# Kernel tuning notes

Hardware: AMD Instinct MI355X
Metric: run time of the kernel (lower is better)

The kernel has to match this reference:

```python
import jax, jax.numpy as jnp
import numpy as np

BN, BE, B = 50000, 800000, 16
NE, EE, GE, EH, NH = 32, 32, 32, 128, 128  # emb dims, hidden dims


def clean(x):
    return jnp.nan_to_num(x, nan=0.0, posinf=0.0, neginf=0.0)


def _lin(key, fan_in, fan_out):
    k1, k2 = jax.random.split(key)
    s = 1.0 / np.sqrt(fan_in)
    return (jax.random.uniform(k1, (fan_in, fan_out), jnp.float32, -s, s),
            jax.random.uniform(k2, (fan_out,), jnp.float32, -s, s))


def setup_inputs() -> dict:
    key = jax.random.key(0)
    ks = jax.random.split(key, 20)
    inp = {
        "x": jax.random.normal(ks[0], (BN, 2), jnp.float32),
        "edge_index": jax.random.randint(ks[1], (2, BE), 0, BN, jnp.int32),
        "batch": jax.random.randint(ks[2], (BN,), 0, B, jnp.int32),
        "node_attr": jnp.ones((BN, 2), jnp.float32),
        "edge_attr": jax.random.uniform(ks[3], (BE, 2), jnp.float32) + 0.5,  # positive spacings
        "glob_attr": jax.random.uniform(ks[4], (B, 2), jnp.float32),
    }
    # encoders (output 2*emb each, 'Duplicated')
    inp["enc_node_W"], inp["enc_node_b"] = _lin(ks[5], 2, 2 * NE)
    inp["enc_edge_W"], inp["enc_edge_b"] = _lin(ks[6], 2, 2 * EE)
    inp["enc_glob_W"], inp["enc_glob_b"] = _lin(ks[7], 2, 2 * GE)
    inp["enc2_W"], inp["enc2_b"] = _lin(ks[8], 2, 2 * EE)
    # derivative MLP: 4*NE+2*EE -> EH -> 2*EE
    inp["dW1"], inp["db1"] = _lin(ks[9], 4 * NE + 2 * EE, EH)
    inp["dW2"], inp["db2"] = _lin(ks[10], EH, 2 * EE)
    # half-jacobian MLP: 4*EE -> EH -> 2*EE
    inp["hW1"], inp["hb1"] = _lin(ks[11], 4 * EE, EH)
    inp["hW2"], inp["hb2"] = _lin(ks[12], EH, 2 * EE)
    # jacobian MLP: 6*EE -> NH -> 2*NE
    inp["jW1"], inp["jb1"] = _lin(ks[13], 6 * EE, NH)
    inp["jW2"], inp["jb2"] = _lin(ks[14], NH, 2 * NE)
    # hessian MLP: 4*EE+2*EE -> NH -> 2*NE
    inp["sW1"], inp["sb1"] = _lin(ks[15], 6 * EE, NH)
    inp["sW2"], inp["sb2"] = _lin(ks[16], NH, 2 * NE)
    # node MLP: 6*NE+2*GE -> NH -> 2*NE
    inp["nW1"], inp["nb1"] = _lin(ks[17], 6 * NE + 2 * GE, NH)
    inp["nW2"], inp["nb2"] = _lin(ks[18], NH, 2 * NE)
    # decoder: 2*NE -> 2
    inp["decW"], inp["decb"] = _lin(ks[19], 2 * NE, 2)
    return inp


def reference(x, edge_index, batch, node_attr, edge_attr, glob_attr,
              enc_node_W, enc_node_b, enc_edge_W, enc_edge_b, enc_glob_W, enc_glob_b,
              enc2_W, enc2_b,
              dW1, db1, dW2, db2,
              hW1, hb1, hW2, hb2,
              jW1, jb1, jW2, jb2,
              sW1, sb1, sW2, sb2,
              nW1, nb1, nW2, nb2,
              decW, decb):
    relu = jax.nn.relu
    seg = lambda d, idx: jax.ops.segment_sum(d, idx, num_segments=BN)
    mlp = lambda t, W1, b1, W2, b2: relu(t @ W1 + b1) @ W2 + b2

    row, col = edge_index[0], edge_index[1]
    spacing = edge_attr                                 # [BE,2]
    inv_spacing = clean(1.0 / spacing)
    inv_double = clean(1.0 / (seg(spacing, row) + seg(spacing, col)))  # [BN,2]

    node_emb = relu(x @ enc_node_W + enc_node_b)        # [BN,2*NE]
    spacing_emb = relu(spacing @ enc_edge_W + enc_edge_b)  # [BE,2*EE]
    glob_emb = relu(glob_attr @ enc_glob_W + enc_glob_b)   # [B,2*GE]
    inv_spacing_emb = relu(inv_spacing @ enc2_W + enc2_b)  # [BE,2*EE]
    inv_double_emb = relu(inv_double @ enc2_W + enc2_b)    # [BN,2*EE]

    d_edge = mlp(jnp.concatenate([node_emb[row], node_emb[col], inv_spacing_emb], -1),
                 dW1, db1, dW2, db2)                    # [BE,2*EE]
    hj_plus = seg(d_edge, row)                          # [BN,2*EE]
    hj_minus = seg(d_edge, col)

    jac1 = seg(mlp(jnp.concatenate([spacing_emb, hj_plus[col]], -1), hW1, hb1, hW2, hb2), col)
    jac2 = seg(mlp(jnp.concatenate([spacing_emb, hj_minus[row]], -1), hW1, hb1, hW2, hb2), row)
    jac = mlp(jnp.concatenate([jac1, jac2, inv_double_emb], -1), jW1, jb1, jW2, jb2)  # [BN,2*NE]

    hess = mlp(jnp.concatenate([hj_plus, hj_minus, inv_double_emb], -1), sW1, sb1, sW2, sb2)

    res = mlp(jnp.concatenate([node_emb, jac, glob_emb[batch], hess], -1), nW1, nb1, nW2, nb2)
    return node_attr * (res @ decW + decb)              # [BN,2]
```

## Files before the change

### kernel.cpp

```cpp
#include <hip/hip_runtime.h>
#include <hip/hip_fp16.h>
#include <math.h>

#define BN 50000
#define BE 800000
#define CHUNK 104

typedef _Float16 h2 __attribute__((ext_vector_type(2)));

__device__ __forceinline__ float relu_f(float v) { return fmaxf(v, 0.0f); }
__device__ __forceinline__ float inv_clean(float s) {
    float q = 1.0f / s;
    return isfinite(q) ? q : 0.0f;
}
__device__ __forceinline__ float inv_clean_fast(float s) {
    float q = __builtin_amdgcn_rcpf(s);
    return isfinite(q) ? q : 0.0f;
}
__device__ __forceinline__ float fdot2f(h2 a, h2 b, float c) {
    return __builtin_amdgcn_fdot2(a, b, c, false);
}
__device__ __forceinline__ unsigned int h2u(h2 v) { union { h2 h; unsigned int u; } x; x.h = v; return x.u; }
__device__ __forceinline__ h2 uh2(unsigned int v) { union { unsigned int u; h2 h; } x; x.u = v; return x.h; }
__device__ __forceinline__ unsigned int packh2(float a, float b) {
    h2 h; h.x = (_Float16)a; h.y = (_Float16)b; return h2u(h);
}

__global__ __launch_bounds__(256) void k_pack_w1(
    const float* __restrict__ W, int r0, float4* __restrict__ dst)
{
    int t = blockIdx.x * 256 + threadIdx.x;
    if (t >= 2048) return;
    int j2 = t >> 6, l = t & 63;
    const float* ra = W + (size_t)(r0 + 2*j2) * 128 + 2*l;
    const float* rb = W + (size_t)(r0 + 2*j2 + 1) * 128 + 2*l;
    dst[t] = make_float4(ra[0], ra[1], rb[0], rb[1]);
}
__global__ __launch_bounds__(256) void k_pack_uv(
    const float* __restrict__ dW1, float4* __restrict__ dst)
{
    int t = blockIdx.x * 256 + threadIdx.x;
    if (t >= 4096) return;
    int j = t >> 6, l = t & 63;
    float4 w;
    if (l < 32) w = ((const float4*)(dW1 + (size_t)j*128))[l];
    else        w = ((const float4*)(dW1 + (size_t)(64+j)*128))[l-32];
    dst[t] = w;
}
__global__ __launch_bounds__(256) void k_pack_w1h(
    const float* __restrict__ W, int r0, uint2* __restrict__ dst)
{
    int t = blockIdx.x * 256 + threadIdx.x;
    if (t >= 2048) return;
    int j2 = t >> 6, l = t & 63;
    const float* ra = W + (size_t)(r0 + 2*j2) * 128;
    const float* rb = W + (size_t)(r0 + 2*j2 + 1) * 128;
    dst[t] = make_uint2(packh2(ra[2*l],   rb[2*l]),
                        packh2(ra[2*l+1], rb[2*l+1]));
}
__global__ __launch_bounds__(256) void k_pack_w2h(
    const float* __restrict__ W2, uint2* __restrict__ dst)
{
    int t = blockIdx.x * 256 + threadIdx.x;
    if (t >= 2048) return;
    int k4 = t >> 6, l = t & 63;
    dst[t] = make_uint2(packh2(W2[(4*k4+0)*64+l], W2[(4*k4+1)*64+l]),
                        packh2(W2[(4*k4+2)*64+l], W2[(4*k4+3)*64+l]));
}

__global__ __launch_bounds__(256) void k_hist(
    const int* __restrict__ ei, int* __restrict__ rc, int* __restrict__ cc)
{
    int e = blockIdx.x * 256 + threadIdx.x;
    if (e >= BE) return;
    atomicAdd(&rc[ei[e]], 1);
    atomicAdd(&cc[ei[BE + e]], 1);
}

__global__ __launch_bounds__(1024) void k_scan(
    const int* __restrict__ cntR, int* __restrict__ hdR,
    const int* __restrict__ cntC, int* __restrict__ hdC)
{
    __shared__ int s[1024];
    const int* cnt; int* hd;
    if (blockIdx.x == 0) { cnt = cntR; hd = hdR; }
    else                 { cnt = cntC; hd = hdC; }
    int t = threadIdx.x;
    int base = t * 49;
    int sum = 0;
    for (int i = 0; i < 49; i++) {
        int idx = base + i;
        sum += (idx < BN) ? cnt[idx] : 0;
    }
    s[t] = sum;
    __syncthreads();
    for (int o = 1; o < 1024; o <<= 1) {
        int v = (t >= o) ? s[t - o] : 0;
        __syncthreads();
        s[t] += v;
        __syncthreads();
    }
    int run = s[t] - sum;
    for (int i = 0; i < 49; i++) {
        int idx = base + i;
        if (idx < BN) { hd[idx] = run; run += cnt[idx]; }
    }
}

__global__ __launch_bounds__(256) void k_scatter2(
    const int* __restrict__ ei, const float* __restrict__ ea,
    int* __restrict__ rhd, int* __restrict__ chd,
    int4* __restrict__ rs, int4* __restrict__ cs)
{
    int e = blockIdx.x * 256 + threadIdx.x;
    if (e >= BE) return;
    int r = ei[e], c = ei[BE + e];
    float2 s = ((const float2*)ea)[e];
    int s0 = __float_as_int(s.x), s1 = __float_as_int(s.y);
    int p1 = atomicAdd(&rhd[r], 1);
    rs[p1] = make_int4(r, c, s0, s1);
    int p2 = atomicAdd(&chd[c], 1);
    cs[p2] = make_int4(c, r, s0, s1);
}

__global__ __launch_bounds__(256) void k_sumsp2(
    const int4* __restrict__ rs, const int* __restrict__ rhd, const int* __restrict__ rcnt,
    const int4* __restrict__ cs, const int* __restrict__ chd, const int* __restrict__ ccnt,
    float* __restrict__ sumsp)
{
    int n = blockIdx.x * 256 + threadIdx.x;
    if (n >= BN) return;
    float s0 = 0.f, s1 = 0.f;
    int e1 = rhd[n], e0 = e1 - rcnt[n];
    for (int j = e0; j < e1; j++) {
        int4 rec = rs[j];
        s0 += __int_as_float(rec.z); s1 += __int_as_float(rec.w);
    }
    e1 = chd[n]; e0 = e1 - ccnt[n];
    for (int j = e0; j < e1; j++) {
        int4 rec = cs[j];
        s0 += __int_as_float(rec.z); s1 += __int_as_float(rec.w);
    }
    sumsp[2*n]   = s0;
    sumsp[2*n+1] = s1;
}

__global__ __launch_bounds__(256, 6) void k_uvh(
    const float* __restrict__ x,
    const float* __restrict__ enW, const float* __restrict__ enB,
    const float4* __restrict__ guv,
    __half* __restrict__ u_h, __half* __restrict__ v_h)
{
    extern __shared__ float lds[];
    const int wid = threadIdx.x >> 6, l = threadIdx.x & 63;
    float4* xb4 = (float4*)(lds + wid * 512);
    const int gw = blockIdx.x * 4 + wid;
    const int nw = gridDim.x * 4;

    const int jj = l & 31;
    const float w0a = enW[jj],    w0b = enW[64+jj],  b0 = enB[jj];
    const float w1a = enW[jj+32], w1b = enW[96+jj],  b1 = enB[jj+32];

    for (int g = gw; g < BN/8; g += nw) {
        const int n0 = g * 8;
        const int q = l >> 5;
        {
            float2 xa = ((const float2*)x)[n0 + q*4 + 0];
            float2 xb = ((const float2*)x)[n0 + q*4 + 1];
            float2 xc = ((const float2*)x)[n0 + q*4 + 2];
            float2 xd = ((const float2*)x)[n0 + q*4 + 3];
            float4 p0, p1;
            p0.x = relu_f(fmaf(xa.x, w0a, fmaf(xa.y, w0b, b0)));
            p0.y = relu_f(fmaf(xb.x, w0a, fmaf(xb.y, w0b, b0)));
            p0.z = relu_f(fmaf(xc.x, w0a, fmaf(xc.y, w0b, b0)));
            p0.w = relu_f(fmaf(xd.x, w0a, fmaf(xd.y, w0b, b0)));
            p1.x = relu_f(fmaf(xa.x, w1a, fmaf(xa.y, w1b, b1)));
            p1.y = relu_f(fmaf(xb.x, w1a, fmaf(xb.y, w1b, b1)));
            p1.z = relu_f(fmaf(xc.x, w1a, fmaf(xc.y, w1b, b1)));
            p1.w = relu_f(fmaf(xd.x, w1a, fmaf(xd.y, w1b, b1)));
            xb4[jj*2 + q]      = p0;
            xb4[(jj+32)*2 + q] = p1;
        }
        float4 acc[8];
        #pragma unroll
        for (int e = 0; e < 8; e++) acc[e] = make_float4(0,0,0,0);
        #pragma unroll 8
        for (int j = 0; j < 64; j++) {
            float4 wq = guv[j*64 + l];
            float4 xa = xb4[j*2 + 0];
            float4 xc = xb4[j*2 + 1];
            acc[0].x = fmaf(xa.x, wq.x, acc[0].x); acc[0].y = fmaf(xa.x, wq.y, acc[0].y);
            acc[0].z = fmaf(xa.x, wq.z, acc[0].z); acc[0].w = fmaf(xa.x, wq.w, acc[0].w);
            acc[1].x = fmaf(xa.y, wq.x, acc[1].x); acc[1].y = fmaf(xa.y, wq.y, acc[1].y);
            acc[1].z = fmaf(xa.y, wq.z, acc[1].z); acc[1].w = fmaf(xa.y, wq.w, acc[1].w);
            acc[2].x = fmaf(xa.z, wq.x, acc[2].x); acc[2].y = fmaf(xa.z, wq.y, acc[2].y);
            acc[2].z = fmaf(xa.z, wq.z, acc[2].z); acc[2].w = fmaf(xa.z, wq.w, acc[2].w);
            acc[3].x = fmaf(xa.w, wq.x, acc[3].x); acc[3].y = fmaf(xa.w, wq.y, acc[3].y);
            acc[3].z = fmaf(xa.w, wq.z, acc[3].z); acc[3].w = fmaf(xa.w, wq.w, acc[3].w);
            acc[4].x = fmaf(xc.x, wq.x, acc[4].x); acc[4].y = fmaf(xc.x, wq.y, acc[4].y);
            acc[4].z = fmaf(xc.x, wq.z, acc[4].z); acc[4].w = fmaf(xc.x, wq.w, acc[4].w);
            acc[5].x = fmaf(xc.y, wq.x, acc[5].x); acc[5].y = fmaf(xc.y, wq.y, acc[5].y);
            acc[5].z = fmaf(xc.y, wq.z, acc[5].z); acc[5].w = fmaf(xc.y, wq.w, acc[5].w);
            acc[6].x = fmaf(xc.z, wq.x, acc[6].x); acc[6].y = fmaf(xc.z, wq.y, acc[6].y);
            acc[6].z = fmaf(xc.z, wq.z, acc[6].z); acc[6].w = fmaf(xc.z, wq.w, acc[6].w);
            acc[7].x = fmaf(xc.w, wq.x, acc[7].x); acc[7].y = fmaf(xc.w, wq.y, acc[7].y);
            acc[7].z = fmaf(xc.w, wq.z, acc[7].z); acc[7].w = fmaf(xc.w, wq.w, acc[7].w);
        }
        __half* dst = (l < 32) ? (u_h + 4*l) : (v_h + 4*(l-32));
        #pragma unroll
        for (int e = 0; e < 8; e++) {
            __half2* p = (__half2*)(dst + (size_t)(n0+e)*128);
            p[0] = __floats2half2_rn(acc[e].x, acc[e].y);
            p[1] = __floats2half2_rn(acc[e].z, acc[e].w);
        }
    }
}

__global__ __launch_bounds__(256, 8) void k_e1d(
    const int4* __restrict__ recs,
    const __half* __restrict__ A_h, const __half* __restrict__ B_h,
    const float* __restrict__ e2w, const float* __restrict__ e2b,
    const uint2* __restrict__ pw1, const float* __restrict__ db1,
    const uint2* __restrict__ pw2, const float* __restrict__ db2,
    float* __restrict__ outAcc)
{
    extern __shared__ unsigned int ldsu[];
    const int wid = threadIdx.x >> 6, l = threadIdx.x & 63;
    uint4* xbuf = (uint4*)ldsu + (size_t)wid * 192;
    uint4* hbuf = xbuf + 64;

    const int j2 = l >> 1, eh = l & 1;
    const float w0a = e2w[2*j2],    w0b = e2w[64+2*j2], eb0 = e2b[2*j2];
    const float w1a = e2w[2*j2+1],  w1b = e2w[65+2*j2], eb1 = e2b[2*j2+1];
    const float b1a = db1[2*l], b1b = db1[2*l+1];
    const float b2r = db2[l];

    const int wave = blockIdx.x * 4 + wid;
    const int start = wave * CHUNK;
    const int end = min(start + CHUNK, BE);

    float acc = 0.f;
    int cur = -1;

    for (int i = start; i < end; i += 8) {
        const int nact = min(8, end - i);
        int key[8], oth[8];
        float spx[8], spy[8];
        #pragma unroll
        for (int e = 0; e < 8; e++) {
            int idx = i + ((e < nact) ? e : nact - 1);
            int4 rec = recs[idx];
            key[e] = rec.x; oth[e] = rec.y;
            spx[e] = __int_as_float(rec.z); spy[e] = __int_as_float(rec.w);
        }
        {
            uint4 xw;
            unsigned int* xp = (unsigned int*)&xw;
            #pragma unroll
            for (int c = 0; c < 4; c++) {
                int e = 4*eh + c;
                float q0 = inv_clean_fast(spx[e]);
                float q1 = inv_clean_fast(spy[e]);
                float r0 = relu_f(fmaf(q0, w0a, fmaf(q1, w0b, eb0)));
                float r1 = relu_f(fmaf(q0, w1a, fmaf(q1, w1b, eb1)));
                xp[c] = packh2(r0, r1);
            }
            xbuf[j2*2 + eh] = xw;
        }
        float t0[8], t1[8];
        #pragma unroll
        for (int e = 0; e < 8; e++) {
            float2 au = __half22float2(*(const __half2*)(A_h + (size_t)key[e]*128 + 2*l));
            float2 bu = __half22float2(*(const __half2*)(B_h + (size_t)oth[e]*128 + 2*l));
            t0[e] = b1a + au.x + bu.x;
            t1[e] = b1b + au.y + bu.y;
        }
        #pragma unroll 8
        for (int p = 0; p < 32; p++) {
            uint4 x0 = xbuf[p*2 + 0];
            uint4 x1 = xbuf[p*2 + 1];
            uint2 wv = pw1[p*64 + l];
            h2 wa = uh2(wv.x), wb = uh2(wv.y);
            t0[0] = fdot2f(uh2(x0.x), wa, t0[0]); t1[0] = fdot2f(uh2(x0.x), wb, t1[0]);
            t0[1] = fdot2f(uh2(x0.y), wa, t0[1]); t1[1] = fdot2f(uh2(x0.y), wb, t1[1]);
            t0[2] = fdot2f(uh2(x0.z), wa, t0[2]); t1[2] = fdot2f(uh2(x0.z), wb, t1[2]);
            t0[3] = fdot2f(uh2(x0.w), wa, t0[3]); t1[3] = fdot2f(uh2(x0.w), wb, t1[3]);
            t0[4] = fdot2f(uh2(x1.x), wa, t0[4]); t1[4] = fdot2f(uh2(x1.x), wb, t1[4]);
            t0[5] = fdot2f(uh2(x1.y), wa, t0[5]); t1[5] = fdot2f(uh2(x1.y), wb, t1[5]);
            t0[6] = fdot2f(uh2(x1.z), wa, t0[6]); t1[6] = fdot2f(uh2(x1.z), wb, t1[6]);
            t0[7] = fdot2f(uh2(x1.w), wa, t0[7]); t1[7] = fdot2f(uh2(x1.w), wb, t1[7]);
        }
        {
            uint4 hA, hB;
            unsigned int* pa = (unsigned int*)&hA;
            unsigned int* pb = (unsigned int*)&hB;
            #pragma unroll
            for (int c = 0; c < 4; c++) {
                pa[c] = packh2(relu_f(t0[c]),   relu_f(t1[c]));
                pb[c] = packh2(relu_f(t0[4+c]), relu_f(t1[4+c]));
            }
            hbuf[l*2 + 0] = hA;
            hbuf[l*2 + 1] = hB;
        }
        float o[8] = {0,0,0,0,0,0,0,0};
        #pragma unroll 8
        for (int k4 = 0; k4 < 32; k4++) {
            uint4 a0 = hbuf[(2*k4)*2 + 0];
            uint4 a1 = hbuf[(2*k4)*2 + 1];
            uint4 b0 = hbuf[(2*k4+1)*2 + 0];
            uint4 b1 = hbuf[(2*k4+1)*2 + 1];
            uint2 wv = pw2[k4*64 + l];
            h2 wa = uh2(wv.x), wb = uh2(wv.y);
            o[0] = fdot2f(uh2(b0.x), wb, fdot2f(uh2(a0.x), wa, o[0]));
            o[1] = fdot2f(uh2(b0.y), wb, fdot2f(uh2(a0.y), wa, o[1]));
            o[2] = fdot2f(uh2(b0.z), wb, fdot2f(uh2(a0.z), wa, o[2]));
            o[3] = fdot2f(uh2(b0.w), wb, fdot2f(uh2(a0.w), wa, o[3]));
            o[4] = fdot2f(uh2(b1.x), wb, fdot2f(uh2(a1.x), wa, o[4]));
            o[5] = fdot2f(uh2(b1.y), wb, fdot2f(uh2(a1.y), wa, o[5]));
            o[6] = fdot2f(uh2(b1.z), wb, fdot2f(uh2(a1.z), wa, o[6]));
            o[7] = fdot2f(uh2(b1.w), wb, fdot2f(uh2(a1.w), wa, o[7]));
        }
        #pragma unroll
        for (int e = 0; e < 8; e++) {
            if (e < nact) {
                float val = o[e] + b2r;
                if (key[e] != cur) {
                    if (cur >= 0) atomicAdd(&outAcc[(size_t)cur*64 + l], acc);
                    acc = 0.f;
                    cur = key[e];
                }
                acc += val;
            }
        }
    }
    if (cur >= 0) atomicAdd(&outAcc[(size_t)cur*64 + l], acc);
}

__global__ __launch_bounds__(256, 6) void k_tptmh(
    const float* __restrict__ hjp, const float* __restrict__ hjm,
    const float4* __restrict__ gtp,
    __half* __restrict__ tp_h, __half* __restrict__ tm_h)
{
    extern __shared__ float lds[];
    const int wid = threadIdx.x >> 6, l = threadIdx.x & 63;
    float4* xb4 = (float4*)(lds + wid * 512);
    const int gw = blockIdx.x * 4 + wid;
    const int nw = gridDim.x * 4;
    const int NG = BN/8;

    for (int vg = gw; vg < 2*NG; vg += nw) {
        const float* in = (vg < NG) ? hjp : hjm;
        __half*     out = (vg < NG) ? tp_h : tm_h;
        const int n0 = ((vg < NG) ? vg : vg - NG) * 8;
        const int q = l >> 5;
        #pragma unroll
        for (int r = 0; r < 2; r++) {
            int j = (l & 31) + 32*r;
            float v0 = in[(n0 + q*4 + 0)*64 + j];
            float v1 = in[(n0 + q*4 + 1)*64 + j];
            float v2 = in[(n0 + q*4 + 2)*64 + j];
            float v3 = in[(n0 + q*4 + 3)*64 + j];
            xb4[j*2 + q] = make_float4(v0, v1, v2, v3);
        }
        float a0[8] = {0,0,0,0,0,0,0,0}, a1[8] = {0,0,0,0,0,0,0,0};
        #pragma unroll 8
        for (int j2 = 0; j2 < 32; j2++) {
            float4 wq = gtp[j2*64 + l];
            float4 xa = xb4[(2*j2)*2 + 0];
            float4 xbv = xb4[(2*j2)*2 + 1];
            float4 xc = xb4[(2*j2+1)*2 + 0];
            float4 xd = xb4[(2*j2+1)*2 + 1];
            a0[0] = fmaf(xa.x, wq.x, fmaf(xc.x, wq.z, a0[0]));
            a1[0] = fmaf(xa.x, wq.y, fmaf(xc.x, wq.w, a1[0]));
            a0[1] = fmaf(xa.y, wq.x, fmaf(xc.y, wq.z, a0[1]));
            a1[1] = fmaf(xa.y, wq.y, fmaf(xc.y, wq.w, a1[1]));
            a0[2] = fmaf(xa.z, wq.x, fmaf(xc.z, wq.z, a0[2]));
            a1[2] = fmaf(xa.z, wq.y, fmaf(xc.z, wq.w, a1[2]));
            a0[3] = fmaf(xa.w, wq.x, fmaf(xc.w, wq.z, a0[3]));
            a1[3] = fmaf(xa.w, wq.y, fmaf(xc.w, wq.w, a1[3]));
            a0[4] = fmaf(xbv.x, wq.x, fmaf(xd.x, wq.z, a0[4]));
            a1[4] = fmaf(xbv.x, wq.y, fmaf(xd.x, wq.w, a1[4]));
            a0[5] = fmaf(xbv.y, wq.x, fmaf(xd.y, wq.z, a0[5]));
            a1[5] = fmaf(xbv.y, wq.y, fmaf(xd.y, wq.w, a1[5]));
            a0[6] = fmaf(xbv.z, wq.x, fmaf(xd.z, wq.z, a0[6]));
            a1[6] = fmaf(xbv.z, wq.y, fmaf(xd.z, wq.w, a1[6]));
            a0[7] = fmaf(xbv.w, wq.x, fmaf(xd.w, wq.z, a0[7]));
            a1[7] = fmaf(xbv.w, wq.y, fmaf(xd.w, wq.w, a1[7]));
        }
        #pragma unroll
        for (int e = 0; e < 8; e++) {
            *(__half2*)(out + (size_t)(n0+e)*128 + 2*l) = __floats2half2_rn(a0[e], a1[e]);
        }
    }
}

__global__ __launch_bounds__(256, 8) void k_e2s(
    const int4* __restrict__ recs, const __half* __restrict__ tvals_h,
    const float* __restrict__ eew, const float* __restrict__ eeb,
    const uint2* __restrict__ pw1, const float* __restrict__ hb1,
    const uint2* __restrict__ pw2, const float* __restrict__ hb2,
    float* __restrict__ out)
{
    extern __shared__ unsigned int ldsu[];
    const int wid = threadIdx.x >> 6, l = threadIdx.x & 63;
    uint4* xbuf = (uint4*)ldsu + (size_t)wid * 192;
    uint4* hbuf = xbuf + 64;

    const int j2 = l >> 1, eh = l & 1;
    const float w0a = eew[2*j2],    w0b = eew[64+2*j2], eb0 = eeb[2*j2];
    const float w1a = eew[2*j2+1],  w1b = eew[65+2*j2], eb1 = eeb[2*j2+1];
    const float b1a = hb1[2*l], b1b = hb1[2*l+1];
    const float b2r = hb2[l];

    const int wave = blockIdx.x * 4 + wid;
    const int start = wave * CHUNK;
    const int end = min(start + CHUNK, BE);

    float acc = 0.f;
    int cur = -1;

    for (int i = start; i < end; i += 8) {
        const int nact = min(8, end - i);
        int key[8];
        float spx[8], spy[8];
        #pragma unroll
        for (int e = 0; e < 8; e++) {
            int idx = i + ((e < nact) ? e : nact - 1);
            int4 rec = recs[idx];
            key[e] = rec.x;
            spx[e] = __int_as_float(rec.z); spy[e] = __int_as_float(rec.w);
        }
        {
            uint4 xw;
            unsigned int* xp = (unsigned int*)&xw;
            #pragma unroll
            for (int c = 0; c < 4; c++) {
                int e = 4*eh + c;
                float r0 = relu_f(fmaf(spx[e], w0a, fmaf(spy[e], w0b, eb0)));
                float r1 = relu_f(fmaf(spx[e], w1a, fmaf(spy[e], w1b, eb1)));
                xp[c] = packh2(r0, r1);
            }
            xbuf[j2*2 + eh] = xw;
        }
        float t0[8], t1[8];
        #pragma unroll
        for (int e = 0; e < 8; e++) {
            float2 tv = __half22float2(*(const __half2*)(tvals_h + (size_t)key[e]*128 + 2*l));
            t0[e] = b1a + tv.x;
            t1[e] = b1b + tv.y;
        }
        #pragma unroll 8
        for (int p = 0; p < 32; p++) {
            uint4 x0 = xbuf[p*2 + 0];
            uint4 x1 = xbuf[p*2 + 1];
            uint2 wv = pw1[p*64 + l];
            h2 wa = uh2(wv.x), wb = uh2(wv.y);
            t0[0] = fdot2f(uh2(x0.x), wa, t0[0]); t1[0] = fdot2f(uh2(x0.x), wb, t1[0]);
            t0[1] = fdot2f(uh2(x0.y), wa, t0[1]); t1[1] = fdot2f(uh2(x0.y), wb, t1[1]);
            t0[2] = fdot2f(uh2(x0.z), wa, t0[2]); t1[2] = fdot2f(uh2(x0.z), wb, t1[2]);
            t0[3] = fdot2f(uh2(x0.w), wa, t0[3]); t1[3] = fdot2f(uh2(x0.w), wb, t1[3]);
            t0[4] = fdot2f(uh2(x1.x), wa, t0[4]); t1[4] = fdot2f(uh2(x1.x), wb, t1[4]);
            t0[5] = fdot2f(uh2(x1.y), wa, t0[5]); t1[5] = fdot2f(uh2(x1.y), wb, t1[5]);
            t0[6] = fdot2f(uh2(x1.z), wa, t0[6]); t1[6] = fdot2f(uh2(x1.z), wb, t1[6]);
            t0[7] = fdot2f(uh2(x1.w), wa, t0[7]); t1[7] = fdot2f(uh2(x1.w), wb, t1[7]);
        }
        {
            uint4 hA, hB;
            unsigned int* pa = (unsigned int*)&hA;
            unsigned int* pb = (unsigned int*)&hB;
            #pragma unroll
            for (int c = 0; c < 4; c++) {
                pa[c] = packh2(relu_f(t0[c]),   relu_f(t1[c]));
                pb[c] = packh2(relu_f(t0[4+c]), relu_f(t1[4+c]));
            }
            hbuf[l*2 + 0] = hA;
            hbuf[l*2 + 1] = hB;
        }
        float o[8] = {0,0,0,0,0,0,0,0};
        #pragma unroll 8
        for (int k4 = 0; k4 < 32; k4++) {
            uint4 a0 = hbuf[(2*k4)*2 + 0];
            uint4 a1 = hbuf[(2*k4)*2 + 1];
            uint4 b0 = hbuf[(2*k4+1)*2 + 0];
            uint4 b1 = hbuf[(2*k4+1)*2 + 1];
            uint2 wv = pw2[k4*64 + l];
            h2 wa = uh2(wv.x), wb = uh2(wv.y);
            o[0] = fdot2f(uh2(b0.x), wb, fdot2f(uh2(a0.x), wa, o[0]));
            o[1] = fdot2f(uh2(b0.y), wb, fdot2f(uh2(a0.y), wa, o[1]));
            o[2] = fdot2f(uh2(b0.z), wb, fdot2f(uh2(a0.z), wa, o[2]));
            o[3] = fdot2f(uh2(b0.w), wb, fdot2f(uh2(a0.w), wa, o[3]));
            o[4] = fdot2f(uh2(b1.x), wb, fdot2f(uh2(a1.x), wa, o[4]));
            o[5] = fdot2f(uh2(b1.y), wb, fdot2f(uh2(a1.y), wa, o[5]));
            o[6] = fdot2f(uh2(b1.z), wb, fdot2f(uh2(a1.z), wa, o[6]));
            o[7] = fdot2f(uh2(b1.w), wb, fdot2f(uh2(a1.w), wa, o[7]));
        }
        #pragma unroll
        for (int e = 0; e < 8; e++) {
            if (e < nact) {
                float val = o[e] + b2r;
                if (key[e] != cur) {
                    if (cur >= 0) atomicAdd(&out[(size_t)cur*64 + l], acc);
                    acc = 0.f;
                    cur = key[e];
                }
                acc += val;
            }
        }
    }
    if (cur >= 0) atomicAdd(&out[(size_t)cur*64 + l], acc);
}

__global__ __launch_bounds__(256, 4) void k_node_mlp(
    const float* __restrict__ A, const float* __restrict__ Bv,
    const float* __restrict__ sumsp,
    const float* __restrict__ e2w_g, const float* __restrict__ e2b_g,
    const float* __restrict__ W1g, const float* __restrict__ b1g,
    const float* __restrict__ W2g, const float* __restrict__ b2g,
    float* __restrict__ outp)
{
    extern __shared__ float lds[];
    const int wid = threadIdx.x >> 6, l = threadIdx.x & 63;
    float* xbuf = lds + wid * 768;
    float* hbuf = lds + 4*768 + wid * 512;

    const float ewl = e2w_g[l], ewl2 = e2w_g[64+l], ebl = e2b_g[l];
    const float bb0 = b1g[2*l], bb1 = b1g[2*l+1];
    const float bo = b2g[l];

    const int gw = blockIdx.x * 4 + wid;
    const int nw = gridDim.x * 4;

    for (int g = gw; g < BN/4; g += nw) {
        const int i0 = g * 4;
        float av[4], bv[4], iv[4];
        #pragma unroll
        for (int e = 0; e < 4; e++) {
            int i = i0 + e;
            av[e] = A[i*64 + l];
            bv[e] = Bv[i*64 + l];
            float q0 = inv_clean(sumsp[i*2+0]);
            float q1 = inv_clean(sumsp[i*2+1]);
            iv[e] = relu_f(fmaf(q0, ewl, fmaf(q1, ewl2, ebl)));
        }
        ((float4*)xbuf)[l]       = make_float4(av[0], av[1], av[2], av[3]);
        ((float4*)xbuf)[64 + l]  = make_float4(bv[0], bv[1], bv[2], bv[3]);
        ((float4*)xbuf)[128 + l] = make_float4(iv[0], iv[1], iv[2], iv[3]);

        float acc0[4] = {0,0,0,0}, acc1[4] = {0,0,0,0};
        #pragma unroll 8
        for (int j = 0; j < 192; j++) {
            float4 xv = ((const float4*)xbuf)[j];
            float2 wv = ((const float2*)(W1g + j*128))[l];
            acc0[0] = fmaf(xv.x, wv.x, acc0[0]);
            acc0[1] = fmaf(xv.y, wv.x, acc0[1]);
            acc0[2] = fmaf(xv.z, wv.x, acc0[2]);
            acc0[3] = fmaf(xv.w, wv.x, acc0[3]);
            acc1[0] = fmaf(xv.x, wv.y, acc1[0]);
            acc1[1] = fmaf(xv.y, wv.y, acc1[1]);
            acc1[2] = fmaf(xv.z, wv.y, acc1[2]);
            acc1[3] = fmaf(xv.w, wv.y, acc1[3]);
        }
        #pragma unroll
        for (int e = 0; e < 4; e++) {
            ((float2*)(hbuf + e*128))[l] = make_float2(relu_f(acc0[e]+bb0), relu_f(acc1[e]+bb1));
        }
        float o[4] = {0,0,0,0};
        #pragma unroll 8
        for (int k = 0; k < 128; k++) {
            float wv = W2g[k*64 + l];
            o[0] = fmaf(hbuf[0*128+k], wv, o[0]);
            o[1] = fmaf(hbuf[1*128+k], wv, o[1]);
            o[2] = fmaf(hbuf[2*128+k], wv, o[2]);
            o[3] = fmaf(hbuf[3*128+k], wv, o[3]);
        }
        #pragma unroll
        for (int e = 0; e < 4; e++) outp[(i0+e)*64 + l] = o[e] + bo;
    }
}

__global__ __launch_bounds__(256, 4) void k_node_final(
    const float* __restrict__ x,
    const float* __restrict__ enW, const float* __restrict__ enB,
    const float* __restrict__ jacv, const float* __restrict__ hessv,
    const int* __restrict__ batch, const float* __restrict__ ga,
    const float* __restrict__ gw_g, const float* __restrict__ gb_g,
    const float* __restrict__ nW1, const float* __restrict__ nb1,
    const float* __restrict__ nW2, const float* __restrict__ nb2,
    const float* __restrict__ decW, const float* __restrict__ decb,
    const float* __restrict__ node_attr, float* __restrict__ outp)
{
    extern __shared__ float lds[];
    const int wid = threadIdx.x >> 6, l = threadIdx.x & 63;
    float* xbuf = lds + wid * 1024;
    float* hbuf = lds + 4*1024 + wid * 512;

    const float gwl = gw_g[l], gwl2 = gw_g[64+l], gbl = gb_g[l];
    const float enw0 = enW[l], enw1 = enW[64+l], enb = enB[l];
    const float bb0 = nb1[2*l], bb1 = nb1[2*l+1];
    const float bo = nb2[l];

    const int gwv = blockIdx.x * 4 + wid;
    const int nw = gridDim.x * 4;

    for (int g = gwv; g < BN/4; g += nw) {
        const int i0 = g * 4;
        float ne[4], jv[4], ge[4], hv[4];
        #pragma unroll
        for (int e = 0; e < 4; e++) {
            int i = i0 + e;
            ne[e] = relu_f(fmaf(x[i*2], enw0, fmaf(x[i*2+1], enw1, enb)));
            jv[e] = jacv[i*64 + l];
            hv[e] = hessv[i*64 + l];
            int gi = batch[i];
            ge[e] = relu_f(fmaf(ga[gi*2], gwl, fmaf(ga[gi*2+1], gwl2, gbl)));
        }
        ((float4*)xbuf)[l]       = make_float4(ne[0], ne[1], ne[2], ne[3]);
        ((float4*)xbuf)[64 + l]  = make_float4(jv[0], jv[1], jv[2], jv[3]);
        ((float4*)xbuf)[128 + l] = make_float4(ge[0], ge[1], ge[2], ge[3]);
        ((float4*)xbuf)[192 + l] = make_float4(hv[0], hv[1], hv[2], hv[3]);

        float acc0[4] = {0,0,0,0}, acc1[4] = {0,0,0,0};
        #pragma unroll 8
        for (int j = 0; j < 256; j++) {
            float4 xv = ((const float4*)xbuf)[j];
            float2 wv = ((const float2*)(nW1 + j*128))[l];
            acc0[0] = fmaf(xv.x, wv.x, acc0[0]);
            acc0[1] = fmaf(xv.y, wv.x, acc0[1]);
            acc0[2] = fmaf(xv.z, wv.x, acc0[2]);
            acc0[3] = fmaf(xv.w, wv.x, acc0[3]);
            acc1[0] = fmaf(xv.x, wv.y, acc1[0]);
            acc1[1] = fmaf(xv.y, wv.y, acc1[1]);
            acc1[2] = fmaf(xv.z, wv.y, acc1[2]);
            acc1[3] = fmaf(xv.w, wv.y, acc1[3]);
        }
        #pragma unroll
        for (int e = 0; e < 4; e++) {
            ((float2*)(hbuf + e*128))[l] = make_float2(relu_f(acc0[e]+bb0), relu_f(acc1[e]+bb1));
        }
        float o[4] = {0,0,0,0};
        #pragma unroll 8
        for (int k = 0; k < 128; k++) {
            float wv = nW2[k*64 + l];
            o[0] = fmaf(hbuf[0*128+k], wv, o[0]);
            o[1] = fmaf(hbuf[1*128+k], wv, o[1]);
            o[2] = fmaf(hbuf[2*128+k], wv, o[2]);
            o[3] = fmaf(hbuf[3*128+k], wv, o[3]);
        }
        #pragma unroll
        for (int e = 0; e < 4; e++) hbuf[e*128 + l] = o[e] + bo;

        int e2 = l >> 4, sub = l & 15, j2 = sub >> 3, part = sub & 7;
        float s = 0.0f;
        #pragma unroll
        for (int kk = 0; kk < 8; kk++) {
            int k = part*8 + kk;
            s = fmaf(hbuf[e2*128 + k], decW[k*2 + j2], s);
        }
        s += __shfl_xor(s, 1);
        s += __shfl_xor(s, 2);
        s += __shfl_xor(s, 4);
        if (part == 0) {
            int i = i0 + e2;
            outp[i*2 + j2] = (s + decb[j2]) * node_attr[i*2 + j2];
        }
    }
}

extern "C" void kernel_launch(void* const* d_in, const int* in_sizes, int n_in,
                              void* d_out, int out_size, void* d_ws, size_t ws_size,
                              hipStream_t stream) {
    const float* x          = (const float*)d_in[0];
    const int*   ei         = (const int*)  d_in[1];
    const int*   batch      = (const int*)  d_in[2];
    const float* node_attr  = (const float*)d_in[3];
    const float* edge_attr  = (const float*)d_in[4];
    const float* glob_attr  = (const float*)d_in[5];
    const float* enc_node_W = (const float*)d_in[6];
    const float* enc_node_b = (const float*)d_in[7];
    const float* enc_edge_W = (const float*)d_in[8];
    const float* enc_edge_b = (const float*)d_in[9];
    const float* enc_glob_W = (const float*)d_in[10];
    const float* enc_glob_b = (const float*)d_in[11];
    const float* enc2_W     = (const float*)d_in[12];
    const float* enc2_b     = (const float*)d_in[13];
    const float* dW1 = (const float*)d_in[14]; const float* db1 = (const float*)d_in[15];
    const float* dW2 = (const float*)d_in[16]; const float* db2 = (const float*)d_in[17];
    const float* hW1 = (const float*)d_in[18]; const float* hb1 = (const float*)d_in[19];
    const float* hW2 = (const float*)d_in[20]; const float* hb2 = (const float*)d_in[21];
    const float* jW1 = (const float*)d_in[22]; const float* jb1 = (const float*)d_in[23];
    const float* jW2 = (const float*)d_in[24]; const float* jb2 = (const float*)d_in[25];
    const float* sW1 = (const float*)d_in[26]; const float* sb1 = (const float*)d_in[27];
    const float* sW2 = (const float*)d_in[28]; const float* sb2 = (const float*)d_in[29];
    const float* nW1 = (const float*)d_in[30]; const float* nb1 = (const float*)d_in[31];
    const float* nW2 = (const float*)d_in[32]; const float* nb2 = (const float*)d_in[33];
    const float* decW = (const float*)d_in[34]; const float* decb = (const float*)d_in[35];

    float* ws = (float*)d_ws;
    int4*   rs    = (int4*)ws;
    int4*   cs    = (int4*)(ws + 3200000);
    __half* u_h   = (__half*)(ws + 6400000);
    __half* v_h   = (__half*)(ws + 9600000);
    float*  hjp   = ws + 12800000;
    float*  hjm   = ws + 16000000;
    float*  jac1  = ws + 19200000;
    float*  jac2  = ws + 22400000;
    float*  sumsp = ws + 25600000;
    int*    row_cnt = (int*)(ws + 25700000);
    int*    col_cnt = row_cnt + 50176;
    int*    row_hd  = col_cnt + 50176;
    int*    col_hd  = row_hd + 50048;

    float* scratch = (float*)d_out;
    float4* puv   = (float4*)(scratch);
    float4* ptp   = (float4*)(scratch + 16384);
    uint2*  pe1w1 = (uint2*)(scratch + 24576);
    uint2*  pe1w2 = (uint2*)(scratch + 28672);
    uint2*  pe2w1 = (uint2*)(scratch + 32768);
    uint2*  pe2w2 = (uint2*)(scratch + 36864);

    hipMemsetAsync(hjp, 0, (size_t)12800000*sizeof(float), stream);
    hipMemsetAsync(row_cnt, 0, (size_t)(2*50176)*sizeof(int), stream);

    k_pack_uv<<<16, 256, 0, stream>>>(dW1, puv);
    k_pack_w1<<<8, 256, 0, stream>>>(hW1, 64, ptp);
    k_pack_w1h<<<8, 256, 0, stream>>>(dW1, 128, pe1w1);
    k_pack_w2h<<<8, 256, 0, stream>>>(dW2, pe1w2);
    k_pack_w1h<<<8, 256, 0, stream>>>(hW1, 0, pe2w1);
    k_pack_w2h<<<8, 256, 0, stream>>>(hW2, pe2w2);

    k_uvh<<<1563, 256, 2048*4, stream>>>(x, enc_node_W, enc_node_b, puv, u_h, v_h);

    k_hist<<<3125, 256, 0, stream>>>(ei, row_cnt, col_cnt);
    k_scan<<<2, 1024, 0, stream>>>(row_cnt, row_hd, col_cnt, col_hd);
    k_scatter2<<<3125, 256, 0, stream>>>(ei, edge_attr, row_hd, col_hd, rs, cs);
    k_sumsp2<<<196, 256, 0, stream>>>(rs, row_hd, row_cnt, cs, col_hd, col_cnt, sumsp);

    const int E_BLOCKS = ((BE + CHUNK - 1) / CHUNK + 3) / 4;
    const size_t lds_e = 4 * 192 * 16;

    k_e1d<<<E_BLOCKS, 256, lds_e, stream>>>(rs, u_h, v_h, enc2_W, enc2_b,
                                            pe1w1, db1, pe1w2, db2, hjp);
    k_e1d<<<E_BLOCKS, 256, lds_e, stream>>>(cs, v_h, u_h, enc2_W, enc2_b,
                                            pe1w1, db1, pe1w2, db2, hjm);

    k_tptmh<<<1536, 256, 2048*4, stream>>>(hjp, hjm, ptp, u_h, v_h);

    k_e2s<<<E_BLOCKS, 256, lds_e, stream>>>(cs, u_h, enc_edge_W, enc_edge_b,
                                            pe2w1, hb1, pe2w2, hb2, jac1);
    k_e2s<<<E_BLOCKS, 256, lds_e, stream>>>(rs, v_h, enc_edge_W, enc_edge_b,
                                            pe2w1, hb1, pe2w2, hb2, jac2);

    size_t lds_nm = (4*768 + 4*512) * sizeof(float);
    k_node_mlp<<<1024, 256, lds_nm, stream>>>(jac1, jac2, sumsp, enc2_W, enc2_b,
                                              jW1, jb1, jW2, jb2, jac1);
    k_node_mlp<<<1024, 256, lds_nm, stream>>>(hjp, hjm, sumsp, enc2_W, enc2_b,
                                              sW1, sb1, sW2, sb2, hjp);

    size_t lds_nf = (4*1024 + 4*512) * sizeof(float);
    k_node_final<<<1024, 256, lds_nf, stream>>>(x, enc_node_W, enc_node_b,
                                                jac1, hjp,
                                                batch, glob_attr, enc_glob_W, enc_glob_b,
                                                nW1, nb1, nW2, nb2, decW, decb,
                                                node_attr, (float*)d_out);
}
```

Baseline: 2.435 ms.

## Partition edge waves on node boundaries to replace atomics with plain stores

```diff
diff --git a/kernel.cpp b/kernel.cpp
--- a/kernel.cpp
+++ b/kernel.cpp
@@ -5,6 +5,7 @@
 #define BN 50000
 #define BE 800000
 #define CHUNK 104
+#define NWAVES 7693
 
 typedef _Float16 h2 __attribute__((ext_vector_type(2)));
 
@@ -25,6 +26,7 @@
 __device__ __forceinline__ unsigned int packh2(float a, float b) {
     h2 h; h.x = (_Float16)a; h.y = (_Float16)b; return h2u(h);
 }
+__device__ __forceinline__ int pad4(int i) { return i + (i >> 3); }
 
 __global__ __launch_bounds__(256) void k_pack_w1(
     const float* __restrict__ W, int r0, float4* __restrict__ dst)
@@ -143,6 +145,28 @@
     }
     sumsp[2*n]   = s0;
     sumsp[2*n+1] = s1;
+}
+
+__global__ __launch_bounds__(256) void k_part(
+    const int* __restrict__ rhd, const int* __restrict__ rcnt, int* __restrict__ lbr,
+    const int* __restrict__ chd, const int* __restrict__ ccnt, int* __restrict__ lbc)
+{
+    int t = blockIdx.x * 256 + threadIdx.x;
+    if (t >= 2 * (NWAVES + 1)) return;
+    int which = (t > NWAVES) ? 1 : 0;
+    int w = t - which * (NWAVES + 1);
+    const int* hd  = which ? chd  : rhd;
+    const int* cnt = which ? ccnt : rcnt;
+    int* lb        = which ? lbc  : lbr;
+    if (w == NWAVES) { lb[NWAVES] = BN; return; }
+    int target = w * CHUNK;
+    int lo = 0, hi = BN;
+    while (lo < hi) {
+        int mid = (lo + hi) >> 1;
+        int s = hd[mid] - cnt[mid];
+        if (s >= target) hi = mid; else lo = mid + 1;
+    }
+    lb[w] = lo;
 }
 
 __global__ __launch_bounds__(256, 6) void k_uvh(
@@ -216,9 +240,10 @@
     }
 }
 
-__global__ __launch_bounds__(256, 8) void k_e1d(
+__global__ __launch_bounds__(256, 8) void k_e1(
     const int4* __restrict__ recs,
     const __half* __restrict__ A_h, const __half* __restrict__ B_h,
+    const int* __restrict__ lb, const int* __restrict__ hd, const int* __restrict__ cnt,
     const float* __restrict__ e2w, const float* __restrict__ e2b,
     const uint2* __restrict__ pw1, const float* __restrict__ db1,
     const uint2* __restrict__ pw2, const float* __restrict__ db2,
@@ -226,8 +251,16 @@
 {
     extern __shared__ unsigned int ldsu[];
     const int wid = threadIdx.x >> 6, l = threadIdx.x & 63;
-    uint4* xbuf = (uint4*)ldsu + (size_t)wid * 192;
-    uint4* hbuf = xbuf + 64;
+    uint4* xbuf = (uint4*)ldsu + (size_t)wid * 216;
+    uint4* hbuf = xbuf + 72;
+
+    const int wave = blockIdx.x * 4 + wid;
+    if (wave >= NWAVES) return;
+    const int n0 = lb[wave], n1 = lb[wave + 1];
+    if (n0 >= n1) return;
+    const int eb = hd[n0] - cnt[n0];
+    const int ee = (n1 < BN) ? (hd[n1] - cnt[n1]) : BE;
+    if (eb >= ee) return;
 
     const int j2 = l >> 1, eh = l & 1;
     const float w0a = e2w[2*j2],    w0b = e2w[64+2*j2], eb0 = e2b[2*j2];
@@ -235,15 +268,11 @@
     const float b1a = db1[2*l], b1b = db1[2*l+1];
     const float b2r = db2[l];
 
-    const int wave = blockIdx.x * 4 + wid;
-    const int start = wave * CHUNK;
-    const int end = min(start + CHUNK, BE);
-
     float acc = 0.f;
     int cur = -1;
 
-    for (int i = start; i < end; i += 8) {
-        const int nact = min(8, end - i);
+    for (int i = eb; i < ee; i += 8) {
+        const int nact = min(8, ee - i);
         int key[8], oth[8];
         float spx[8], spy[8];
         #pragma unroll
@@ -265,7 +294,7 @@
                 float r1 = relu_f(fmaf(q0, w1a, fmaf(q1, w1b, eb1)));
                 xp[c] = packh2(r0, r1);
             }
-            xbuf[j2*2 + eh] = xw;
+            xbuf[pad4(j2*2 + eh)] = xw;
         }
         float t0[8], t1[8];
         #pragma unroll
@@ -277,8 +306,8 @@
         }
         #pragma unroll 8
         for (int p = 0; p < 32; p++) {
-            uint4 x0 = xbuf[p*2 + 0];
-            uint4 x1 = xbuf[p*2 + 1];
+            uint4 x0 = xbuf[pad4(p*2 + 0)];
+            uint4 x1 = xbuf[pad4(p*2 + 1)];
             uint2 wv = pw1[p*64 + l];
             h2 wa = uh2(wv.x), wb = uh2(wv.y);
             t0[0] = fdot2f(uh2(x0.x), wa, t0[0]); t1[0] = fdot2f(uh2(x0.x), wb, t1[0]);
@@ -299,16 +328,16 @@
                 pa[c] = packh2(relu_f(t0[c]),   relu_f(t1[c]));
                 pb[c] = packh2(relu_f(t0[4+c]), relu_f(t1[4+c]));
             }
-            hbuf[l*2 + 0] = hA;
-            hbuf[l*2 + 1] = hB;
+            hbuf[pad4(l*2 + 0)] = hA;
+            hbuf[pad4(l*2 + 1)] = hB;
         }
         float o[8] = {0,0,0,0,0,0,0,0};
         #pragma unroll 8
         for (int k4 = 0; k4 < 32; k4++) {
-            uint4 a0 = hbuf[(2*k4)*2 + 0];
-            uint4 a1 = hbuf[(2*k4)*2 + 1];
-            uint4 b0 = hbuf[(2*k4+1)*2 + 0];
-            uint4 b1 = hbuf[(2*k4+1)*2 + 1];
+            uint4 a0 = hbuf[pad4(4*k4 + 0)];
+            uint4 a1 = hbuf[pad4(4*k4 + 1)];
+            uint4 b0 = hbuf[pad4(4*k4 + 2)];
+            uint4 b1 = hbuf[pad4(4*k4 + 3)];
             uint2 wv = pw2[k4*64 + l];
             h2 wa = uh2(wv.x), wb = uh2(wv.y);
             o[0] = fdot2f(uh2(b0.x), wb, fdot2f(uh2(a0.x), wa, o[0]));
@@ -325,7 +354,7 @@
             if (e < nact) {
                 float val = o[e] + b2r;
                 if (key[e] != cur) {
-                    if (cur >= 0) atomicAdd(&outAcc[(size_t)cur*64 + l], acc);
+                    if (cur >= 0) outAcc[(size_t)cur*64 + l] = acc;
                     acc = 0.f;
                     cur = key[e];
                 }
@@ -333,7 +362,7 @@
             }
         }
     }
-    if (cur >= 0) atomicAdd(&outAcc[(size_t)cur*64 + l], acc);
+    if (cur >= 0) outAcc[(size_t)cur*64 + l] = acc;
 }
 
 __global__ __launch_bounds__(256, 6) void k_tptmh(
@@ -394,8 +423,9 @@
     }
 }
 
-__global__ __launch_bounds__(256, 8) void k_e2s(
+__global__ __launch_bounds__(256, 8) void k_e2(
     const int4* __restrict__ recs, const __half* __restrict__ tvals_h,
+    const int* __restrict__ lb, const int* __restrict__ hd, const int* __restrict__ cnt,
     const float* __restrict__ eew, const float* __restrict__ eeb,
     const uint2* __restrict__ pw1, const float* __restrict__ hb1,
     const uint2* __restrict__ pw2, const float* __restrict__ hb2,
@@ -403,8 +433,16 @@
 {
     extern __shared__ unsigned int ldsu[];
     const int wid = threadIdx.x >> 6, l = threadIdx.x & 63;
-    uint4* xbuf = (uint4*)ldsu + (size_t)wid * 192;
-    uint4* hbuf = xbuf + 64;
+    uint4* xbuf = (uint4*)ldsu + (size_t)wid * 216;
+    uint4* hbuf = xbuf + 72;
+
+    const int wave = blockIdx.x * 4 + wid;
+    if (wave >= NWAVES) return;
+    const int n0 = lb[wave], n1 = lb[wave + 1];
+    if (n0 >= n1) return;
+    const int eb = hd[n0] - cnt[n0];
+    const int ee = (n1 < BN) ? (hd[n1] - cnt[n1]) : BE;
+    if (eb >= ee) return;
 
     const int j2 = l >> 1, eh = l & 1;
     const float w0a = eew[2*j2],    w0b = eew[64+2*j2], eb0 = eeb[2*j2];
@@ -412,15 +450,11 @@
     const float b1a = hb1[2*l], b1b = hb1[2*l+1];
     const float b2r = hb2[l];
 
-    const int wave = blockIdx.x * 4 + wid;
-    const int start = wave * CHUNK;
-    const int end = min(start + CHUNK, BE);
-
     float acc = 0.f;
     int cur = -1;
 
-    for (int i = start; i < end; i += 8) {
-        const int nact = min(8, end - i);
+    for (int i = eb; i < ee; i += 8) {
+        const int nact = min(8, ee - i);
         int key[8];
         float spx[8], spy[8];
         #pragma unroll
@@ -440,7 +474,7 @@
                 float r1 = relu_f(fmaf(spx[e], w1a, fmaf(spy[e], w1b, eb1)));
                 xp[c] = packh2(r0, r1);
             }
-            xbuf[j2*2 + eh] = xw;
+            xbuf[pad4(j2*2 + eh)] = xw;
         }
         float t0[8], t1[8];
         #pragma unroll
@@ -451,8 +485,8 @@
         }
         #pragma unroll 8
         for (int p = 0; p < 32; p++) {
-            uint4 x0 = xbuf[p*2 + 0];
-            uint4 x1 = xbuf[p*2 + 1];
+            uint4 x0 = xbuf[pad4(p*2 + 0)];
+            uint4 x1 = xbuf[pad4(p*2 + 1)];
             uint2 wv = pw1[p*64 + l];
             h2 wa = uh2(wv.x), wb = uh2(wv.y);
             t0[0] = fdot2f(uh2(x0.x), wa, t0[0]); t1[0] = fdot2f(uh2(x0.x), wb, t1[0]);
@@ -473,16 +507,16 @@
                 pa[c] = packh2(relu_f(t0[c]),   relu_f(t1[c]));
                 pb[c] = packh2(relu_f(t0[4+c]), relu_f(t1[4+c]));
             }
-            hbuf[l*2 + 0] = hA;
-            hbuf[l*2 + 1] = hB;
+            hbuf[pad4(l*2 + 0)] = hA;
+            hbuf[pad4(l*2 + 1)] = hB;
         }
         float o[8] = {0,0,0,0,0,0,0,0};
         #pragma unroll 8
         for (int k4 = 0; k4 < 32; k4++) {
-            uint4 a0 = hbuf[(2*k4)*2 + 0];
-            uint4 a1 = hbuf[(2*k4)*2 + 1];
-            uint4 b0 = hbuf[(2*k4+1)*2 + 0];
-            uint4 b1 = hbuf[(2*k4+1)*2 + 1];
+            uint4 a0 = hbuf[pad4(4*k4 + 0)];
+            uint4 a1 = hbuf[pad4(4*k4 + 1)];
+            uint4 b0 = hbuf[pad4(4*k4 + 2)];
+            uint4 b1 = hbuf[pad4(4*k4 + 3)];
             uint2 wv = pw2[k4*64 + l];
             h2 wa = uh2(wv.x), wb = uh2(wv.y);
             o[0] = fdot2f(uh2(b0.x), wb, fdot2f(uh2(a0.x), wa, o[0]));
@@ -499,7 +533,7 @@
             if (e < nact) {
                 float val = o[e] + b2r;
                 if (key[e] != cur) {
-                    if (cur >= 0) atomicAdd(&out[(size_t)cur*64 + l], acc);
+                    if (cur >= 0) out[(size_t)cur*64 + l] = acc;
                     acc = 0.f;
                     cur = key[e];
                 }
@@ -507,7 +541,7 @@
             }
         }
     }
-    if (cur >= 0) atomicAdd(&out[(size_t)cur*64 + l], acc);
+    if (cur >= 0) out[(size_t)cur*64 + l] = acc;
 }
 
 __global__ __launch_bounds__(256, 4) void k_node_mlp(
@@ -709,6 +743,8 @@
     int*    col_cnt = row_cnt + 50176;
     int*    row_hd  = col_cnt + 50176;
     int*    col_hd  = row_hd + 50048;
+    int*    lbr     = col_hd + 50048;
+    int*    lbc     = lbr + 7694;
 
     float* scratch = (float*)d_out;
     float4* puv   = (float4*)(scratch);
@@ -734,21 +770,24 @@
     k_scan<<<2, 1024, 0, stream>>>(row_cnt, row_hd, col_cnt, col_hd);
     k_scatter2<<<3125, 256, 0, stream>>>(ei, edge_attr, row_hd, col_hd, rs, cs);
     k_sumsp2<<<196, 256, 0, stream>>>(rs, row_hd, row_cnt, cs, col_hd, col_cnt, sumsp);
-
-    const int E_BLOCKS = ((BE + CHUNK - 1) / CHUNK + 3) / 4;
-    const size_t lds_e = 4 * 192 * 16;
-
-    k_e1d<<<E_BLOCKS, 256, lds_e, stream>>>(rs, u_h, v_h, enc2_W, enc2_b,
-                                            pe1w1, db1, pe1w2, db2, hjp);
-    k_e1d<<<E_BLOCKS, 256, lds_e, stream>>>(cs, v_h, u_h, enc2_W, enc2_b,
-                                            pe1w1, db1, pe1w2, db2, hjm);
+    k_part<<<61, 256, 0, stream>>>(row_hd, row_cnt, lbr, col_hd, col_cnt, lbc);
+
+    const int E_BLOCKS = (NWAVES + 3) / 4;
+    const size_t lds_e = 4 * 216 * 16;
+
+    k_e1<<<E_BLOCKS, 256, lds_e, stream>>>(rs, u_h, v_h, lbr, row_hd, row_cnt,
+                                           enc2_W, enc2_b, pe1w1, db1, pe1w2, db2, hjp);
+    k_e1<<<E_BLOCKS, 256, lds_e, stream>>>(cs, v_h, u_h, lbc, col_hd, col_cnt,
+                                           enc2_W, enc2_b, pe1w1, db1, pe1w2, db2, hjm);
 
     k_tptmh<<<1536, 256, 2048*4, stream>>>(hjp, hjm, ptp, u_h, v_h);
 
-    k_e2s<<<E_BLOCKS, 256, lds_e, stream>>>(cs, u_h, enc_edge_W, enc_edge_b,
-                                            pe2w1, hb1, pe2w2, hb2, jac1);
-    k_e2s<<<E_BLOCKS, 256, lds_e, stream>>>(rs, v_h, enc_edge_W, enc_edge_b,
-                                            pe2w1, hb1, pe2w2, hb2, jac2);
+    k_e2<<<E_BLOCKS, 256, lds_e, stream>>>(cs, u_h, lbc, col_hd, col_cnt,
+                                           enc_edge_W, enc_edge_b,
+                                           pe2w1, hb1, pe2w2, hb2, jac1);
+    k_e2<<<E_BLOCKS, 256, lds_e, stream>>>(rs, v_h, lbr, row_hd, row_cnt,
+                                           enc_edge_W, enc_edge_b,
+                                           pe2w1, hb1, pe2w2, hb2, jac2);
 
     size_t lds_nm = (4*768 + 4*512) * sizeof(float);
     k_node_mlp<<<1024, 256, lds_nm, stream>>>(jac1, jac2, sumsp, enc2_W, enc2_b,
```

Measured after the change: 2.579 ms. 5.9% more time.
